# Performance work log

Measured on AMD Instinct MI355X. Metric: run time of the kernel, lower is better.

## Reference

```python
import jax, jax.numpy as jnp
import numpy as np

EMBED_DIM = 1024
NUM_HEADS = 16
HEAD_DIM = EMBED_DIM // NUM_HEADS


def setup_inputs() -> dict:
    key = jax.random.key(0)
    k_x, k_wqkv, k_bqkv, k_wout, k_bout = jax.random.split(key, 5)
    s = 1.0 / np.sqrt(EMBED_DIM)
    return {
        "x": jax.random.normal(k_x, (2, 2048, EMBED_DIM), dtype=jnp.float32),
        "w_qkv": jax.random.uniform(k_wqkv, (EMBED_DIM, 3 * EMBED_DIM), jnp.float32, -s, s),
        "b_qkv": jax.random.uniform(k_bqkv, (3 * EMBED_DIM,), jnp.float32, -s, s),
        "w_out": jax.random.uniform(k_wout, (EMBED_DIM, EMBED_DIM), jnp.float32, -s, s),
        "b_out": jax.random.uniform(k_bout, (EMBED_DIM,), jnp.float32, -s, s),
    }


def reference(x, w_qkv, b_qkv, w_out, b_out):
    B, S, D = x.shape
    H, Hd = NUM_HEADS, HEAD_DIM
    # qkv projection, then per-head chunk: layout matches torch view(B,S,H,3*Hd).chunk(3,-1)
    qkv = (x @ w_qkv + b_qkv).reshape(B, S, H, 3, Hd)  # [B,S,H,3,Hd]
    q = qkv[..., 0, :]  # [B,S,H,Hd]
    k = qkv[..., 1, :]
    v = qkv[..., 2, :]
    scale = 1.0 / np.sqrt(Hd).astype(np.float32)
    scores = jnp.einsum("bqhd,bkhd->bhqk", q, k) * scale  # [B,H,S,S]
    probs = jax.nn.softmax(scores, axis=-1)
    out = jnp.einsum("bhqk,bkhd->bqhd", probs, v).reshape(B, S, D)
    return out @ w_out + b_out
```

## Files before the change

### kernel.cpp

```cpp
#include <hip/hip_runtime.h>
#include <hip/hip_bf16.h>


typedef __bf16 bf16;
typedef __bf16 bf16x8 __attribute__((ext_vector_type(8)));
typedef float  f32x4  __attribute__((ext_vector_type(4)));
typedef float  f32x16 __attribute__((ext_vector_type(16)));
typedef unsigned int uint;
typedef unsigned int uint2v __attribute__((ext_vector_type(2)));

__device__ __forceinline__ void gload_lds16(const void* g, void* l) {
  __builtin_amdgcn_global_load_lds(
      (const __attribute__((address_space(1))) unsigned int*)g,
      (__attribute__((address_space(3))) unsigned int*)l, 16, 0, 0);
}

__device__ __forceinline__ uint pkbf16(float lo, float hi) {
  union { bf16 h[2]; uint u; } t;
  t.h[0] = (bf16)lo; t.h[1] = (bf16)hi;
  return t.u;
}

__device__ __forceinline__ void pl32swapu(uint& a, uint& b) {
  uint2v r = __builtin_amdgcn_permlane32_swap(a, b, false, false);
  a = r.x; b = r.y;
}
__device__ __forceinline__ void pl32swapf(float& a, float& b) {
  uint ua = __builtin_bit_cast(uint, a), ub = __builtin_bit_cast(uint, b);
  pl32swapu(ua, ub);
  a = __builtin_bit_cast(float, ua); b = __builtin_bit_cast(float, ub);
}

__global__ __launch_bounds__(256) void k_prep(const float* __restrict__ x,
                                              const float* __restrict__ w_qkv,
                                              const float* __restrict__ w_out,
                                              bf16* __restrict__ xb,
                                              bf16* __restrict__ wqT,
                                              bf16* __restrict__ woT) {
  __shared__ float tile[32][33];
  const int b = blockIdx.x;
  const int tid = threadIdx.x;
  if (b < 2048) {
    int i = (b * 256 + tid) * 8;
    float4 a = *(const float4*)(x + i);
    float4 c = *(const float4*)(x + i + 4);
    bf16x8 o;
    o[0] = (bf16)a.x; o[1] = (bf16)a.y; o[2] = (bf16)a.z; o[3] = (bf16)a.w;
    o[4] = (bf16)c.x; o[5] = (bf16)c.y; o[6] = (bf16)c.z; o[7] = (bf16)c.w;
    *(bf16x8*)(xb + i) = o;
    return;
  }
  const bool perm = (b < 5120);
  const float* in = perm ? w_qkv : w_out;
  bf16* out = perm ? wqT : woT;
  const int N = perm ? 3072 : 1024;
  int idx = perm ? (b - 2048) : (b - 5120);
  int gx = perm ? (idx % 96) : (idx % 32);
  int gy = perm ? (idx / 96) : (idx / 32);
  int n0 = gx * 32, k0 = gy * 32;
  int tx = tid & 31, ty = tid >> 5;
#pragma unroll
  for (int i = 0; i < 4; i++)
    tile[ty + i * 8][tx] = in[(size_t)(k0 + ty + i * 8) * N + n0 + tx];
  __syncthreads();
#pragma unroll
  for (int i = 0; i < 4; i++) {
    int n = n0 + ty + i * 8;
    int row = n;
    if (perm) {
      int rem = n % 192;
      row = (rem >> 6) * 1024 + (n / 192) * 64 + (rem & 63);
    }
    out[(size_t)row * 1024 + k0 + tx] = (bf16)tile[tx][ty + i * 8];
  }
}

template<int BM, int BN>
__device__ __forceinline__ void gemm_tile(const bf16* __restrict__ A, const bf16* __restrict__ B,
                                          int K, int m0, int n0,
                                          bf16* As, bf16* Bs, f32x4 acc[BM / 32][BN / 32]) {
  const int tid  = threadIdx.x;
  const int lane = tid & 63;
  const int wr   = (tid >> 7) & 1;
  const int wc   = (tid >> 6) & 1;
  constexpr int LA = BM / 64, LB = BN / 64;
  auto stage = [&](int k0v, int b) {
#pragma unroll
    for (int i = 0; i < LA; i++) {
      int row = i * 64 + (tid >> 2);
      int sw  = (tid & 3) ^ (row & 3);
      gload_lds16(A + (size_t)(m0 + row) * K + k0v + sw * 8, (char*)As + b * (BM * 64) + i * 4096 + tid * 16);
    }
#pragma unroll
    for (int i = 0; i < LB; i++) {
      int row = i * 64 + (tid >> 2);
      int sw  = (tid & 3) ^ (row & 3);
      gload_lds16(B + (size_t)(n0 + row) * K + k0v + sw * 8, (char*)Bs + b * (BN * 64) + i * 4096 + tid * 16);
    }
  };
  const int nk = K / 32;
  stage(0, 0); stage(32, 1); stage(64, 2);
  for (int t = 0; t < nk; t++) {
    if (t < nk - 2) {
      if constexpr (LA + LB == 4) asm volatile("s_waitcnt vmcnt(8)" ::: "memory");
      else                        asm volatile("s_waitcnt vmcnt(6)" ::: "memory");
    } else if (t < nk - 1) {
      if constexpr (LA + LB == 4) asm volatile("s_waitcnt vmcnt(4)" ::: "memory");
      else                        asm volatile("s_waitcnt vmcnt(3)" ::: "memory");
    } else {
      asm volatile("s_waitcnt vmcnt(0)" ::: "memory");
    }
    __builtin_amdgcn_s_barrier();
    asm volatile("" ::: "memory");
    if (t + 3 < nk) stage((t + 3) * 32, (t + 3) & 3);
    const int cur = t & 3;
    bf16x8 af[BM / 32], bfr[BN / 32];
#pragma unroll
    for (int r = 0; r < BM / 32; r++) {
      int ra = wr * (BM / 2) + r * 16 + (lane & 15);
      af[r]  = *(const bf16x8*)((const char*)As + cur * (BM * 64) + ra * 64 + ((((lane >> 4) << 4)) ^ ((ra & 3) << 4)));
    }
#pragma unroll
    for (int c = 0; c < BN / 32; c++) {
      int rb = wc * (BN / 2) + c * 16 + (lane & 15);
      bfr[c] = *(const bf16x8*)((const char*)Bs + cur * (BN * 64) + rb * 64 + ((((lane >> 4) << 4)) ^ ((rb & 3) << 4)));
    }
#pragma unroll
    for (int r = 0; r < BM / 32; r++)
#pragma unroll
      for (int c = 0; c < BN / 32; c++)
        acc[r][c] = __builtin_amdgcn_mfma_f32_16x16x32_bf16(af[r], bfr[c], acc[r][c], 0, 0, 0);
    asm volatile("" ::: "memory");
  }
}

__global__ __launch_bounds__(512, 2) void k_gemm_qkv(const bf16* __restrict__ A, const bf16* __restrict__ Bt,
                                                     const float* __restrict__ bias,
                                                     bf16* __restrict__ qb, bf16* __restrict__ kb,
                                                     bf16* __restrict__ vtb) {
  __shared__ char GS[131072];
  const int tid  = threadIdx.x;
  const int lane = tid & 63;
  const int wave = tid >> 6;
  const int wr   = wave >> 2;
  const int wc   = wave & 3;
  const int l = blockIdx.x;
  const int swz = (l & 7) * 24 + (l >> 3);
  const int m0 = (swz / 12) * 256, n0 = (swz % 12) * 256;
  const int K = 1024;

  f32x4 acc[8][4];
  f32x4 zero = {0.f, 0.f, 0.f, 0.f};
#pragma unroll
  for (int ms = 0; ms < 8; ms++)
#pragma unroll
    for (int ns = 0; ns < 4; ns++) acc[ms][ns] = zero;

  const int ccs = tid & 7;
  int rA[2], rB[2];
  {
    int lr0 = tid >> 3;
    rA[0] = lr0;
    rB[0] = (lr0 & 31) + ((lr0 >> 5) << 6);
    int lr1 = 64 + lr0;
    rA[1] = (lr1 & 63) + 128;
    rB[1] = (lr1 & 31) + ((lr1 >> 5) << 6);
  }
  const bf16* Agp[2]; const bf16* Bgp[2];
  int Alo[2], Blo[2];
#pragma unroll
  for (int j = 0; j < 2; j++) {
    Agp[j] = A  + (size_t)(m0 + rA[j]) * K + (ccs ^ (rA[j] & 7)) * 8;
    Alo[j] = rA[j] * 128 + ccs * 16;
    Bgp[j] = Bt + (size_t)(n0 + rB[j]) * K + (ccs ^ (rB[j] & 7)) * 8;
    Blo[j] = rB[j] * 128 + ccs * 16;
  }
  auto stA = [&](int t, int h) {
    int b = t & 1;
#pragma unroll
    for (int j = 0; j < 2; j++)
      gload_lds16(Agp[j] + (size_t)(h * 64) * K + t * 64, GS + b * 32768 + Alo[j] + h * 8192);
  };
  auto stB = [&](int t, int h) {
    int b = t & 1;
#pragma unroll
    for (int j = 0; j < 2; j++)
      gload_lds16(Bgp[j] + (size_t)(h * 32) * K + t * 64, GS + 65536 + b * 32768 + Blo[j] + h * 4096);
  };

  bf16x8 af[4][2], bf0[2][2], bf1[2][2];
  auto rdA = [&](const char* Ab, int mh) {
#pragma unroll
    for (int ms = 0; ms < 4; ms++)
#pragma unroll
      for (int ks = 0; ks < 2; ks++) {
        int row = wr * 128 + (mh * 4 + ms) * 16 + (lane & 15);
        int ch = (ks * 4 + (lane >> 4)) ^ (row & 7);
        af[ms][ks] = *(const bf16x8*)(Ab + row * 128 + ch * 16);
      }
  };
  auto rdB = [&](const char* Bb, int nh, bf16x8 (&bfx)[2][2]) {
#pragma unroll
    for (int ns = 0; ns < 2; ns++)
#pragma unroll
      for (int ks = 0; ks < 2; ks++) {
        int row = wc * 64 + (nh * 2 + ns) * 16 + (lane & 15);
        int ch = (ks * 4 + (lane >> 4)) ^ (row & 7);
        bfx[ns][ks] = *(const bf16x8*)(Bb + row * 128 + ch * 16);
      }
  };
  auto mm = [&](int mh, int nh, bf16x8 (&bfx)[2][2]) {
    __builtin_amdgcn_s_setprio(1);
#pragma unroll
    for (int ks = 0; ks < 2; ks++)
#pragma unroll
      for (int ms = 0; ms < 4; ms++)
#pragma unroll
        for (int ns = 0; ns < 2; ns++)
          acc[mh * 4 + ms][nh * 2 + ns] =
              __builtin_amdgcn_mfma_f32_16x16x32_bf16(af[ms][ks], bfx[ns][ks],
                                                      acc[mh * 4 + ms][nh * 2 + ns], 0, 0, 0);
    __builtin_amdgcn_s_setprio(0);
  };

#define BARRIER do { asm volatile("" ::: "memory"); __builtin_amdgcn_s_barrier(); \
                     asm volatile("" ::: "memory"); } while (0)

  stA(0, 0); stB(0, 0); stB(0, 1); stA(0, 1);
  stA(1, 0); stB(1, 0); stB(1, 1);
  asm volatile("s_waitcnt vmcnt(6)" ::: "memory");
  __builtin_amdgcn_s_barrier();
  asm volatile("" ::: "memory");

  for (int I = 0; I < 8; I++) {
    const int T = 2 * I;
    const char* Ab0 = GS;
    const char* Bb0 = GS + 65536;
    const char* Ab1 = GS + 32768;
    const char* Bb1 = GS + 65536 + 32768;
    const bool m2 = (T + 2 < 16), m3 = (T + 3 < 16);

    rdA(Ab0, 0); rdB(Bb0, 0, bf0);
    stA(T + 1, 1);
    BARRIER;
    mm(0, 0, bf0);

    rdB(Bb0, 1, bf1);
    if (m2) stA(T + 2, 0);
    BARRIER;
    mm(0, 1, bf1);

    rdA(Ab0, 1);
    if (m2) stB(T + 2, 0);
    BARRIER;
    mm(1, 0, bf0);

    if (m2) {
      stB(T + 2, 1);
      asm volatile("s_waitcnt vmcnt(6)" ::: "memory");
    } else {
      asm volatile("s_waitcnt vmcnt(0)" ::: "memory");
    }
    __builtin_amdgcn_s_barrier();
    asm volatile("" ::: "memory");
    mm(1, 1, bf1);

    rdA(Ab1, 0); rdB(Bb1, 0, bf0);
    if (m2) stA(T + 2, 1);
    BARRIER;
    mm(0, 0, bf0);

    rdB(Bb1, 1, bf1);
    if (m3) stA(T + 3, 0);
    BARRIER;
    mm(0, 1, bf1);

    rdA(Ab1, 1);
    if (m3) stB(T + 3, 0);
    BARRIER;
    mm(1, 0, bf0);

    if (m3) {
      stB(T + 3, 1);
      asm volatile("s_waitcnt vmcnt(6)" ::: "memory");
    } else {
      asm volatile("s_waitcnt vmcnt(0)" ::: "memory");
    }
    __builtin_amdgcn_s_barrier();
    asm volatile("" ::: "memory");
    mm(1, 1, bf1);
  }
#undef BARRIER

  const int group = n0 >> 10;
  const int hb = (n0 & 1023) >> 6;
  const int b_ = m0 >> 11;
  const float QSs = 0.125f * 1.4426950408889634f;
  char* TL = GS;

  if (group < 2) {
#pragma unroll
    for (int ms = 0; ms < 8; ms++) {
      int mloc = wr * 128 + ms * 16 + ((lane >> 4) << 2);
#pragma unroll
      for (int ns = 0; ns < 4; ns++) {
        int nloc = wc * 64 + ns * 16 + (lane & 15);
        int np = n0 + nloc;
        float bv = bias[((np & 1023) >> 6) * 192 + group * 64 + (np & 63)];
#pragma unroll
        for (int g = 0; g < 4; g++) {
          float v = acc[ms][ns][g] + bv;
          if (group == 0) v *= QSs;
          int m = mloc + g;
          int byte = m * 512 + ((((nloc >> 3) ^ (m & 7)) << 4) | ((nloc & 7) << 1));
          *(bf16*)(TL + byte) = (bf16)v;
        }
      }
    }
    __syncthreads();
    bf16* dst = (group == 0) ? qb : kb;
#pragma unroll
    for (int it = 0; it < 16; it++) {
      int cid = it * 512 + tid;
      int row = cid >> 5, cc = cid & 31;
      int hh = hb + (cc >> 3), ck = cc & 7;
      bf16x8 v8 = *(const bf16x8*)(TL + row * 512 + ((cc ^ (row & 7)) << 4));
      *(bf16x8*)(dst + ((size_t)(b_ * 16 + hh) * 2048 + (m0 & 2047) + row) * 64 + ck * 8) = v8;
    }
  } else {
#pragma unroll
    for (int ms = 0; ms < 8; ms++) {
      int mloc = wr * 128 + ms * 16 + ((lane >> 4) << 2);
#pragma unroll
      for (int ns = 0; ns < 4; ns++) {
        int nloc = wc * 64 + ns * 16 + (lane & 15);
        int np = n0 + nloc;
        float bv = bias[((np & 1023) >> 6) * 192 + 2 * 64 + (np & 63)];
#pragma unroll
        for (int g = 0; g < 4; g++) {
          float v = acc[ms][ns][g] + bv;
          int m = mloc + g;
          int byte = nloc * 512 + ((((m >> 3) ^ (nloc & 7)) << 4) | ((m & 7) << 1));
          *(bf16*)(TL + byte) = (bf16)v;
        }
      }
    }
    __syncthreads();
#pragma unroll
    for (int it = 0; it < 16; it++) {
      int cid = it * 512 + tid;
      int row = cid >> 5, mc = cid & 31;
      int hh = hb + (row >> 6), dd = row & 63;
      bf16x8 v8 = *(const bf16x8*)(TL + row * 512 + ((mc ^ (row & 7)) << 4));
      *(bf16x8*)(vtb + ((size_t)(b_ * 16 + hh) * 64 + dd) * 2048 + (m0 & 2047) + mc * 8) = v8;
    }
  }
}

__global__ __launch_bounds__(256) void k_gemm_out(const bf16* __restrict__ A, const bf16* __restrict__ Bt,
                                                  const float* __restrict__ bias,
                                                  float* __restrict__ out) {
  __shared__ bf16 As[4 * 64 * 32];
  __shared__ bf16 Bs[4 * 128 * 32];
  const int l = blockIdx.x;
  const int swz = (l & 7) * 64 + (l >> 3);
  int m0 = (swz >> 3) * 64, n0 = (swz & 7) * 128;
  f32x4 zero = {0.f, 0.f, 0.f, 0.f};
  f32x4 acc[2][4];
#pragma unroll
  for (int r = 0; r < 2; r++)
#pragma unroll
    for (int c = 0; c < 4; c++) acc[r][c] = zero;
  gemm_tile<64, 128>(A, Bt, 1024, m0, n0, As, Bs, acc);
  const int lane = threadIdx.x & 63;
  const int wr = (threadIdx.x >> 7) & 1, wc = (threadIdx.x >> 6) & 1;
#pragma unroll
  for (int r = 0; r < 2; r++) {
    int mbase = m0 + wr * 32 + r * 16 + ((lane >> 4) << 2);
#pragma unroll
    for (int c = 0; c < 4; c++) {
      int n = n0 + wc * 64 + c * 16 + (lane & 15);
      float bv = bias[n];
#pragma unroll
      for (int g = 0; g < 4; g++)
        out[(size_t)(mbase + g) * 1024 + n] = acc[r][c][g] + bv;
    }
  }
}

__global__ __launch_bounds__(512, 2) void k_attn(const bf16* __restrict__ qb, const bf16* __restrict__ kb,
                                                 const bf16* __restrict__ vtb, bf16* __restrict__ ob) {
  __shared__ char SMEM[147456];
  const int tid  = threadIdx.x;
  const int lane = tid & 63;
  const int wave = tid >> 6;
  const int qp   = wave & 3;
  const int half = wave >> 2;
  const int ln31 = lane & 31;
  const int g    = lane >> 5;

  int l = blockIdx.x;
  int x = l & 7, j = l >> 3;
  int qt = j & 7;
  int bh = x * 4 + (j >> 3);

  const int q0 = qt * 256 + qp * 64;

  bf16x8 qfa[4], qfb[4];
  {
    const bf16* qpa = qb + ((size_t)bh * 2048 + q0 + ln31) * 64 + g * 8;
    const bf16* qpb = qb + ((size_t)bh * 2048 + q0 + 32 + ln31) * 64 + g * 8;
#pragma unroll
    for (int dc = 0; dc < 4; dc++) {
      qfa[dc] = *(const bf16x8*)(qpa + dc * 16);
      qfb[dc] = *(const bf16x8*)(qpb + dc * 16);
    }
  }

  const f32x16 z16 = 0.f;
  f32x16 Oa0 = 0.f, Oa1 = 0.f, Ob0 = 0.f, Ob1 = 0.f;
  float lacc_a[4] = {0.f, 0.f, 0.f, 0.f};
  float lacc_b[4] = {0.f, 0.f, 0.f, 0.f};

  const int rbo = ln31 * 144 + (g << 4);
  const char* kbs = SMEM + half * 9216 + rbo;
  const char* vbs = SMEM + 18432 + half * 9216 + rbo;

  const int c1 = tid, r1 = c1 / 9, cc1 = c1 % 9;
  const int of1 = (cc1 == 8 ? 0 : cc1) * 8;
  const bf16* kg0a = kb  + ((size_t)bh * 2048 +        r1) * 64 + of1;
  const bf16* kg1a = kb  + ((size_t)bh * 2048 + 1024 + r1) * 64 + of1;
  const bf16* vg0a = vtb + ((size_t)bh * 64 + r1) * 2048 +        of1;
  const bf16* vg1a = vtb + ((size_t)bh * 64 + r1) * 2048 + 1024 + of1;
  const int se = tid >> 6;
  const int ce = 512 + (tid & 63), re = ce / 9, cce = ce % 9;
  const int ofe = (cce == 8 ? 0 : cce) * 8;
  const bf16* gext =
      (se == 0) ? kb  + ((size_t)bh * 2048 +        re) * 64 + ofe :
      (se == 1) ? kb  + ((size_t)bh * 2048 + 1024 + re) * 64 + ofe :
      (se == 2) ? vtb + ((size_t)bh * 64 + re) * 2048 +        ofe :
                  vtb + ((size_t)bh * 64 + re) * 2048 + 1024 + ofe;
  const size_t gadv = (se < 2) ? 4096 : 64;
  const int eoff = se * 9216 + ce * 16;

  auto stage = [&](int t, int s) {
    char* bs = SMEM + s * 36864;
    gload_lds16(kg0a + (size_t)t * 4096, bs +         c1 * 16);
    gload_lds16(kg1a + (size_t)t * 4096, bs + 9216  + c1 * 16);
    gload_lds16(vg0a + t * 64,           bs + 18432 + c1 * 16);
    gload_lds16(vg1a + t * 64,           bs + 27648 + c1 * 16);
    if (tid < 256) gload_lds16(gext + (size_t)t * gadv, bs + eoff);
  };

  auto smx = [&](f32x16& sv, bf16x8& f0, bf16x8& f1, float (&lc)[4]) {
#pragma unroll
    for (int r = 0; r < 16; r++) sv[r] = __builtin_amdgcn_exp2f(sv[r]);
#pragma unroll
    for (int r = 0; r < 4; r++)
      lc[r] += (sv[r] + sv[r + 4]) + (sv[r + 8] + sv[r + 12]);
    uint a0 = pkbf16(sv[0], sv[1]), a1 = pkbf16(sv[2], sv[3]);
    uint a2 = pkbf16(sv[4], sv[5]), a3 = pkbf16(sv[6], sv[7]);
    pl32swapu(a0, a2); pl32swapu(a1, a3);
    union { uint w[4]; bf16x8 v; } pa;
    pa.w[0] = a0; pa.w[1] = a1; pa.w[2] = a2; pa.w[3] = a3;
    f0 = pa.v;
    uint b0 = pkbf16(sv[8], sv[9]),  b1 = pkbf16(sv[10], sv[11]);
    uint b2 = pkbf16(sv[12], sv[13]), b3 = pkbf16(sv[14], sv[15]);
    pl32swapu(b0, b2); pl32swapu(b1, b3);
    union { uint w[4]; bf16x8 v; } pb;
    pb.w[0] = b0; pb.w[1] = b1; pb.w[2] = b2; pb.w[3] = b3;
    f1 = pb.v;
  };

  auto pv_chunk = [&](const char* Vb, int cb, bf16x8 f0a, bf16x8 f1a, bf16x8 f0b, bf16x8 f1b) {
    bf16x8 v0 = *(const bf16x8*)(Vb + cb);
    bf16x8 v1 = *(const bf16x8*)(Vb + 4608 + cb);
    Oa0 = __builtin_amdgcn_mfma_f32_32x32x16_bf16(v0, f0a, Oa0, 0, 0, 0);
    Ob0 = __builtin_amdgcn_mfma_f32_32x32x16_bf16(v0, f0b, Ob0, 0, 0, 0);
    Oa1 = __builtin_amdgcn_mfma_f32_32x32x16_bf16(v1, f0a, Oa1, 0, 0, 0);
    Ob1 = __builtin_amdgcn_mfma_f32_32x32x16_bf16(v1, f0b, Ob1, 0, 0, 0);
    v0 = *(const bf16x8*)(Vb + cb + 32);
    v1 = *(const bf16x8*)(Vb + 4608 + cb + 32);
    Oa0 = __builtin_amdgcn_mfma_f32_32x32x16_bf16(v0, f1a, Oa0, 0, 0, 0);
    Ob0 = __builtin_amdgcn_mfma_f32_32x32x16_bf16(v0, f1b, Ob0, 0, 0, 0);
    Oa1 = __builtin_amdgcn_mfma_f32_32x32x16_bf16(v1, f1a, Oa1, 0, 0, 0);
    Ob1 = __builtin_amdgcn_mfma_f32_32x32x16_bf16(v1, f1b, Ob1, 0, 0, 0);
  };

  bf16x8 hf0a, hf1a, hf0b, hf1b;

  stage(0, 0);
  stage(1, 1);
  for (int t = 0; t < 16; t++) {
    if (t + 1 < 16) {
      if (wave < 4) asm volatile("s_waitcnt vmcnt(5)" ::: "memory");
      else          asm volatile("s_waitcnt vmcnt(4)" ::: "memory");
    } else {
      asm volatile("s_waitcnt vmcnt(0)" ::: "memory");
    }
    __builtin_amdgcn_s_barrier();
    asm volatile("" ::: "memory");
    if (t + 2 < 16) stage(t + 2, (t + 2) & 3);

    const char* Kb = kbs + (t & 3) * 36864;
    const char* Vb = vbs + (t & 3) * 36864;

    if (half && t) {
      const char* Vp = vbs + ((t + 3) & 3) * 36864;
      __builtin_amdgcn_s_setprio(1);
      pv_chunk(Vp, 64, hf0a, hf1a, hf0b, hf1b);
      __builtin_amdgcn_s_setprio(0);
    }

    f32x16 sAa, sAb, sBa, sBb;
    __builtin_amdgcn_s_setprio(1);
    {
      bf16x8 kA = *(const bf16x8*)(Kb + 0);
      bf16x8 kB = *(const bf16x8*)(Kb + 4608);
      sAa = __builtin_amdgcn_mfma_f32_32x32x16_bf16(kA, qfa[0], z16, 0, 0, 0);
      sAb = __builtin_amdgcn_mfma_f32_32x32x16_bf16(kA, qfb[0], z16, 0, 0, 0);
      sBa = __builtin_amdgcn_mfma_f32_32x32x16_bf16(kB, qfa[0], z16, 0, 0, 0);
      sBb = __builtin_amdgcn_mfma_f32_32x32x16_bf16(kB, qfb[0], z16, 0, 0, 0);
    }
#pragma unroll
    for (int dc = 1; dc < 4; dc++) {
      bf16x8 kA = *(const bf16x8*)(Kb + dc * 32);
      bf16x8 kB = *(const bf16x8*)(Kb + 4608 + dc * 32);
      sAa = __builtin_amdgcn_mfma_f32_32x32x16_bf16(kA, qfa[dc], sAa, 0, 0, 0);
      sAb = __builtin_amdgcn_mfma_f32_32x32x16_bf16(kA, qfb[dc], sAb, 0, 0, 0);
      sBa = __builtin_amdgcn_mfma_f32_32x32x16_bf16(kB, qfa[dc], sBa, 0, 0, 0);
      sBb = __builtin_amdgcn_mfma_f32_32x32x16_bf16(kB, qfb[dc], sBb, 0, 0, 0);
    }
    __builtin_amdgcn_s_setprio(0);

    bf16x8 fa0, fa1, fb0, fb1;
    smx(sAa, fa0, fa1, lacc_a);
    smx(sAb, fb0, fb1, lacc_b);
    __builtin_amdgcn_s_setprio(1);
    pv_chunk(Vb, 0, fa0, fa1, fb0, fb1);
    __builtin_amdgcn_s_setprio(0);
    if (half) {
      smx(sBa, hf0a, hf1a, lacc_a);
      smx(sBb, hf0b, hf1b, lacc_b);
    } else {
      smx(sBa, fa0, fa1, lacc_a);
      smx(sBb, fb0, fb1, lacc_b);
      __builtin_amdgcn_s_setprio(1);
      pv_chunk(Vb, 64, fa0, fa1, fb0, fb1);
      __builtin_amdgcn_s_setprio(0);
    }
    asm volatile("" ::: "memory");
  }
  if (half) {
    pv_chunk(vbs + 3 * 36864, 64, hf0a, hf1a, hf0b, hf1b);
  }

  float l_ra = (lacc_a[0] + lacc_a[1]) + (lacc_a[2] + lacc_a[3]);
  { float o = l_ra; pl32swapf(l_ra, o); l_ra += o; }
  float l_rb = (lacc_b[0] + lacc_b[1]) + (lacc_b[2] + lacc_b[3]);
  { float o = l_rb; pl32swapf(l_rb, o); l_rb += o; }

  float* Opart = (float*)SMEM;
  float* LsA   = (float*)(SMEM + 69632);
  float* LsB   = (float*)(SMEM + 70144);
  __syncthreads();
  if (half == 1) {
    float* my = Opart + (qp * 64 + lane) * 68;
#pragma unroll
    for (int c = 0; c < 4; c++) {
      *(f32x4*)(my +      c * 4) = f32x4{Oa0[c*4], Oa0[c*4+1], Oa0[c*4+2], Oa0[c*4+3]};
      *(f32x4*)(my + 16 + c * 4) = f32x4{Oa1[c*4], Oa1[c*4+1], Oa1[c*4+2], Oa1[c*4+3]};
      *(f32x4*)(my + 32 + c * 4) = f32x4{Ob0[c*4], Ob0[c*4+1], Ob0[c*4+2], Ob0[c*4+3]};
      *(f32x4*)(my + 48 + c * 4) = f32x4{Ob1[c*4], Ob1[c*4+1], Ob1[c*4+2], Ob1[c*4+3]};
    }
    if (lane < 32) { LsA[qp * 32 + ln31] = l_ra; LsB[qp * 32 + ln31] = l_rb; }
  }
  __syncthreads();
  float inva = 0.f, invb = 0.f;
  if (half == 0) {
    const float* pr = Opart + (qp * 64 + lane) * 68;
#pragma unroll
    for (int c = 0; c < 4; c++) {
      f32x4 a0 = *(const f32x4*)(pr +      c * 4);
      f32x4 a1 = *(const f32x4*)(pr + 16 + c * 4);
      f32x4 b0 = *(const f32x4*)(pr + 32 + c * 4);
      f32x4 b1 = *(const f32x4*)(pr + 48 + c * 4);
#pragma unroll
      for (int k = 0; k < 4; k++) {
        Oa0[c*4+k] += a0[k]; Oa1[c*4+k] += a1[k];
        Ob0[c*4+k] += b0[k]; Ob1[c*4+k] += b1[k];
      }
    }
    inva = 1.0f / (l_ra + LsA[qp * 32 + ln31]);
    invb = 1.0f / (l_rb + LsB[qp * 32 + ln31]);
  }
  __syncthreads();
  bf16 (*Os)[64][72] = reinterpret_cast<bf16 (*)[64][72]>(SMEM);
  if (half == 0) {
#pragma unroll
    for (int r = 0; r < 16; r++) {
      int d0 = (r & 3) + 8 * (r >> 2) + 4 * g;
      Os[qp][ln31][d0]           = (bf16)(Oa0[r] * inva);
      Os[qp][ln31][d0 + 32]      = (bf16)(Oa1[r] * inva);
      Os[qp][32 + ln31][d0]      = (bf16)(Ob0[r] * invb);
      Os[qp][32 + ln31][d0 + 32] = (bf16)(Ob1[r] * invb);
    }
  }
  __syncthreads();
  {
    int b_ = bh >> 4, h = bh & 15;
#pragma unroll
    for (int it = 0; it < 4; it++) {
      int cid = it * 512 + tid;
      int row256 = cid >> 3, c = cid & 7;
      int qpp = row256 >> 6, row = row256 & 63;
      bf16x8 v8o = *(const bf16x8*)&Os[qpp][row][c * 8];
      *(bf16x8*)(ob + ((size_t)(b_ * 2048 + qt * 256 + qpp * 64 + row)) * 1024 + h * 64 + c * 8) = v8o;
    }
  }
}

extern "C" void kernel_launch(void* const* d_in, const int* in_sizes, int n_in,
                              void* d_out, int out_size, void* d_ws, size_t ws_size,
                              hipStream_t stream) {
  const float* x     = (const float*)d_in[0];
  const float* w_qkv = (const float*)d_in[1];
  const float* b_qkv = (const float*)d_in[2];
  const float* w_out = (const float*)d_in[3];
  const float* b_out = (const float*)d_in[4];
  float* out = (float*)d_out;

  char* ws = (char*)d_ws;
  bf16* xb  = (bf16*)ws;
  bf16* wqT = (bf16*)(ws + (8ull  << 20));
  bf16* woT = (bf16*)(ws + (14ull << 20));
  bf16* qb  = (bf16*)(ws + (16ull << 20));
  bf16* kb  = (bf16*)(ws + (24ull << 20));
  bf16* vtb = (bf16*)(ws + (32ull << 20));

  k_prep<<<6144, 256, 0, stream>>>(x, w_qkv, w_out, xb, wqT, woT);
  k_gemm_qkv<<<192, 512, 0, stream>>>(xb, wqT, b_qkv, qb, kb, vtb);
  k_attn<<<256, 512, 0, stream>>>(qb, kb, vtb, xb);
  k_gemm_out<<<512, 256, 0, stream>>>(xb, woT, b_out, out);
}
```

Before: 104.7 us.

## Store K/V in MFMA fragment order and load directly from global in attention

```diff
diff --git a/kernel.cpp b/kernel.cpp
--- a/kernel.cpp
+++ b/kernel.cpp
@@ -136,8 +136,8 @@
 
 __global__ __launch_bounds__(512, 2) void k_gemm_qkv(const bf16* __restrict__ A, const bf16* __restrict__ Bt,
                                                      const float* __restrict__ bias,
-                                                     bf16* __restrict__ qb, bf16* __restrict__ kb,
-                                                     bf16* __restrict__ vtb) {
+                                                     bf16* __restrict__ qb, char* __restrict__ kf,
+                                                     char* __restrict__ vf) {
   __shared__ char GS[131072];
   const int tid  = threadIdx.x;
   const int lane = tid & 63;
@@ -295,6 +295,7 @@
   const int group = n0 >> 10;
   const int hb = (n0 & 1023) >> 6;
   const int b_ = m0 >> 11;
+  const int kt0 = (m0 & 2047) >> 5;
   const float QSs = 0.125f * 1.4426950408889634f;
   char* TL = GS;
 
@@ -318,14 +319,30 @@
       }
     }
     __syncthreads();
-    bf16* dst = (group == 0) ? qb : kb;
-#pragma unroll
-    for (int it = 0; it < 16; it++) {
-      int cid = it * 512 + tid;
-      int row = cid >> 5, cc = cid & 31;
-      int hh = hb + (cc >> 3), ck = cc & 7;
-      bf16x8 v8 = *(const bf16x8*)(TL + row * 512 + ((cc ^ (row & 7)) << 4));
-      *(bf16x8*)(dst + ((size_t)(b_ * 16 + hh) * 2048 + (m0 & 2047) + row) * 64 + ck * 8) = v8;
+    if (group == 0) {
+#pragma unroll
+      for (int it = 0; it < 16; it++) {
+        int cid = it * 512 + tid;
+        int row = cid >> 5, cc = cid & 31;
+        int hh = hb + (cc >> 3), ck = cc & 7;
+        bf16x8 v8 = *(const bf16x8*)(TL + row * 512 + ((cc ^ (row & 7)) << 4));
+        *(bf16x8*)(qb + ((size_t)(b_ * 16 + hh) * 2048 + (m0 & 2047) + row) * 64 + ck * 8) = v8;
+      }
+    } else {
+#pragma unroll
+      for (int it = 0; it < 16; it++) {
+        int cid = it * 512 + tid;
+        int hh = cid >> 11;
+        int ktl = (cid >> 8) & 7;
+        int dc = (cid >> 6) & 3;
+        int gg = (cid >> 5) & 1;
+        int ln = cid & 31;
+        int row = ktl * 32 + ln;
+        int cc = hh * 8 + dc * 2 + gg;
+        bf16x8 v8 = *(const bf16x8*)(TL + row * 512 + ((cc ^ (row & 7)) << 4));
+        *(bf16x8*)(kf + ((size_t)(b_ * 16 + hb + hh) * 64 + kt0 + ktl) * 4096
+                      + (dc * 2 + gg) * 512 + ln * 16) = v8;
+      }
     }
   } else {
 #pragma unroll
@@ -349,10 +366,17 @@
 #pragma unroll
     for (int it = 0; it < 16; it++) {
       int cid = it * 512 + tid;
-      int row = cid >> 5, mc = cid & 31;
-      int hh = hb + (row >> 6), dd = row & 63;
+      int hh = cid >> 11;
+      int ktl = (cid >> 8) & 7;
+      int kc = (cid >> 7) & 1;
+      int dt = (cid >> 6) & 1;
+      int gg = (cid >> 5) & 1;
+      int ln = cid & 31;
+      int row = hh * 64 + dt * 32 + ln;
+      int mc = ktl * 4 + kc * 2 + gg;
       bf16x8 v8 = *(const bf16x8*)(TL + row * 512 + ((mc ^ (row & 7)) << 4));
-      *(bf16x8*)(vtb + ((size_t)(b_ * 16 + hh) * 64 + dd) * 2048 + (m0 & 2047) + mc * 8) = v8;
+      *(bf16x8*)(vf + ((size_t)(b_ * 16 + hb + hh) * 64 + kt0 + ktl) * 4096
+                    + ((kc * 2 + dt) * 2 + gg) * 512 + ln * 16) = v8;
     }
   }
 }
@@ -388,9 +412,9 @@
   }
 }
 
-__global__ __launch_bounds__(512, 2) void k_attn(const bf16* __restrict__ qb, const bf16* __restrict__ kb,
-                                                 const bf16* __restrict__ vtb, bf16* __restrict__ ob) {
-  __shared__ char SMEM[147456];
+__global__ __launch_bounds__(512, 2) void k_attn(const bf16* __restrict__ qb, const char* __restrict__ kf,
+                                                 const char* __restrict__ vf, bf16* __restrict__ ob) {
+  __shared__ char SMEM[73728];
   const int tid  = threadIdx.x;
   const int lane = tid & 63;
   const int wave = tid >> 6;
@@ -422,35 +446,9 @@
   float lacc_a[4] = {0.f, 0.f, 0.f, 0.f};
   float lacc_b[4] = {0.f, 0.f, 0.f, 0.f};
 
-  const int rbo = ln31 * 144 + (g << 4);
-  const char* kbs = SMEM + half * 9216 + rbo;
-  const char* vbs = SMEM + 18432 + half * 9216 + rbo;
-
-  const int c1 = tid, r1 = c1 / 9, cc1 = c1 % 9;
-  const int of1 = (cc1 == 8 ? 0 : cc1) * 8;
-  const bf16* kg0a = kb  + ((size_t)bh * 2048 +        r1) * 64 + of1;
-  const bf16* kg1a = kb  + ((size_t)bh * 2048 + 1024 + r1) * 64 + of1;
-  const bf16* vg0a = vtb + ((size_t)bh * 64 + r1) * 2048 +        of1;
-  const bf16* vg1a = vtb + ((size_t)bh * 64 + r1) * 2048 + 1024 + of1;
-  const int se = tid >> 6;
-  const int ce = 512 + (tid & 63), re = ce / 9, cce = ce % 9;
-  const int ofe = (cce == 8 ? 0 : cce) * 8;
-  const bf16* gext =
-      (se == 0) ? kb  + ((size_t)bh * 2048 +        re) * 64 + ofe :
-      (se == 1) ? kb  + ((size_t)bh * 2048 + 1024 + re) * 64 + ofe :
-      (se == 2) ? vtb + ((size_t)bh * 64 + re) * 2048 +        ofe :
-                  vtb + ((size_t)bh * 64 + re) * 2048 + 1024 + ofe;
-  const size_t gadv = (se < 2) ? 4096 : 64;
-  const int eoff = se * 9216 + ce * 16;
-
-  auto stage = [&](int t, int s) {
-    char* bs = SMEM + s * 36864;
-    gload_lds16(kg0a + (size_t)t * 4096, bs +         c1 * 16);
-    gload_lds16(kg1a + (size_t)t * 4096, bs + 9216  + c1 * 16);
-    gload_lds16(vg0a + t * 64,           bs + 18432 + c1 * 16);
-    gload_lds16(vg1a + t * 64,           bs + 27648 + c1 * 16);
-    if (tid < 256) gload_lds16(gext + (size_t)t * gadv, bs + eoff);
-  };
+  const int lb = (g * 32 + ln31) * 16;
+  const char* Kp = kf + (size_t)bh * 262144 + (half * 32) * 4096 + lb;
+  const char* Vp = vf + (size_t)bh * 262144 + (half * 32) * 4096 + lb;
 
   auto smx = [&](f32x16& sv, bf16x8& f0, bf16x8& f1, float (&lc)[4]) {
 #pragma unroll
@@ -472,87 +470,49 @@
     f1 = pb.v;
   };
 
-  auto pv_chunk = [&](const char* Vb, int cb, bf16x8 f0a, bf16x8 f1a, bf16x8 f0b, bf16x8 f1b) {
-    bf16x8 v0 = *(const bf16x8*)(Vb + cb);
-    bf16x8 v1 = *(const bf16x8*)(Vb + 4608 + cb);
-    Oa0 = __builtin_amdgcn_mfma_f32_32x32x16_bf16(v0, f0a, Oa0, 0, 0, 0);
-    Ob0 = __builtin_amdgcn_mfma_f32_32x32x16_bf16(v0, f0b, Ob0, 0, 0, 0);
-    Oa1 = __builtin_amdgcn_mfma_f32_32x32x16_bf16(v1, f0a, Oa1, 0, 0, 0);
-    Ob1 = __builtin_amdgcn_mfma_f32_32x32x16_bf16(v1, f0b, Ob1, 0, 0, 0);
-    v0 = *(const bf16x8*)(Vb + cb + 32);
-    v1 = *(const bf16x8*)(Vb + 4608 + cb + 32);
-    Oa0 = __builtin_amdgcn_mfma_f32_32x32x16_bf16(v0, f1a, Oa0, 0, 0, 0);
-    Ob0 = __builtin_amdgcn_mfma_f32_32x32x16_bf16(v0, f1b, Ob0, 0, 0, 0);
-    Oa1 = __builtin_amdgcn_mfma_f32_32x32x16_bf16(v1, f1a, Oa1, 0, 0, 0);
-    Ob1 = __builtin_amdgcn_mfma_f32_32x32x16_bf16(v1, f1b, Ob1, 0, 0, 0);
-  };
-
-  bf16x8 hf0a, hf1a, hf0b, hf1b;
-
-  stage(0, 0);
-  stage(1, 1);
-  for (int t = 0; t < 16; t++) {
-    if (t + 1 < 16) {
-      if (wave < 4) asm volatile("s_waitcnt vmcnt(5)" ::: "memory");
-      else          asm volatile("s_waitcnt vmcnt(4)" ::: "memory");
-    } else {
-      asm volatile("s_waitcnt vmcnt(0)" ::: "memory");
-    }
-    __builtin_amdgcn_s_barrier();
-    asm volatile("" ::: "memory");
-    if (t + 2 < 16) stage(t + 2, (t + 2) & 3);
-
-    const char* Kb = kbs + (t & 3) * 36864;
-    const char* Vb = vbs + (t & 3) * 36864;
-
-    if (half && t) {
-      const char* Vp = vbs + ((t + 3) & 3) * 36864;
-      __builtin_amdgcn_s_setprio(1);
-      pv_chunk(Vp, 64, hf0a, hf1a, hf0b, hf1b);
-      __builtin_amdgcn_s_setprio(0);
-    }
-
-    f32x16 sAa, sAb, sBa, sBb;
+  bf16x8 k0 = *(const bf16x8*)(Kp +    0);
+  bf16x8 k1 = *(const bf16x8*)(Kp + 1024);
+  bf16x8 k2 = *(const bf16x8*)(Kp + 2048);
+  bf16x8 k3 = *(const bf16x8*)(Kp + 3072);
+
+  for (int ss = 0; ss < 32; ss++, Kp += 4096, Vp += 4096) {
+    bf16x8 v00 = *(const bf16x8*)(Vp +    0);
+    bf16x8 v01 = *(const bf16x8*)(Vp + 1024);
+    bf16x8 v10 = *(const bf16x8*)(Vp + 2048);
+    bf16x8 v11 = *(const bf16x8*)(Vp + 3072);
+    bf16x8 n0 = *(const bf16x8*)(Kp + 4096);
+    bf16x8 n1 = *(const bf16x8*)(Kp + 5120);
+    bf16x8 n2 = *(const bf16x8*)(Kp + 6144);
+    bf16x8 n3 = *(const bf16x8*)(Kp + 7168);
+
+    f32x16 sa, sb;
     __builtin_amdgcn_s_setprio(1);
-    {
-      bf16x8 kA = *(const bf16x8*)(Kb + 0);
-      bf16x8 kB = *(const bf16x8*)(Kb + 4608);
-      sAa = __builtin_amdgcn_mfma_f32_32x32x16_bf16(kA, qfa[0], z16, 0, 0, 0);
-      sAb = __builtin_amdgcn_mfma_f32_32x32x16_bf16(kA, qfb[0], z16, 0, 0, 0);
-      sBa = __builtin_amdgcn_mfma_f32_32x32x16_bf16(kB, qfa[0], z16, 0, 0, 0);
-      sBb = __builtin_amdgcn_mfma_f32_32x32x16_bf16(kB, qfb[0], z16, 0, 0, 0);
-    }
-#pragma unroll
-    for (int dc = 1; dc < 4; dc++) {
-      bf16x8 kA = *(const bf16x8*)(Kb + dc * 32);
-      bf16x8 kB = *(const bf16x8*)(Kb + 4608 + dc * 32);
-      sAa = __builtin_amdgcn_mfma_f32_32x32x16_bf16(kA, qfa[dc], sAa, 0, 0, 0);
-      sAb = __builtin_amdgcn_mfma_f32_32x32x16_bf16(kA, qfb[dc], sAb, 0, 0, 0);
-      sBa = __builtin_amdgcn_mfma_f32_32x32x16_bf16(kB, qfa[dc], sBa, 0, 0, 0);
-      sBb = __builtin_amdgcn_mfma_f32_32x32x16_bf16(kB, qfb[dc], sBb, 0, 0, 0);
-    }
+    sa = __builtin_amdgcn_mfma_f32_32x32x16_bf16(k0, qfa[0], z16, 0, 0, 0);
+    sb = __builtin_amdgcn_mfma_f32_32x32x16_bf16(k0, qfb[0], z16, 0, 0, 0);
+    sa = __builtin_amdgcn_mfma_f32_32x32x16_bf16(k1, qfa[1], sa, 0, 0, 0);
+    sb = __builtin_amdgcn_mfma_f32_32x32x16_bf16(k1, qfb[1], sb, 0, 0, 0);
+    sa = __builtin_amdgcn_mfma_f32_32x32x16_bf16(k2, qfa[2], sa, 0, 0, 0);
+    sb = __builtin_amdgcn_mfma_f32_32x32x16_bf16(k2, qfb[2], sb, 0, 0, 0);
+    sa = __builtin_amdgcn_mfma_f32_32x32x16_bf16(k3, qfa[3], sa, 0, 0, 0);
+    sb = __builtin_amdgcn_mfma_f32_32x32x16_bf16(k3, qfb[3], sb, 0, 0, 0);
     __builtin_amdgcn_s_setprio(0);
 
     bf16x8 fa0, fa1, fb0, fb1;
-    smx(sAa, fa0, fa1, lacc_a);
-    smx(sAb, fb0, fb1, lacc_b);
+    smx(sa, fa0, fa1, lacc_a);
+    smx(sb, fb0, fb1, lacc_b);
+
     __builtin_amdgcn_s_setprio(1);
-    pv_chunk(Vb, 0, fa0, fa1, fb0, fb1);
+    Oa0 = __builtin_amdgcn_mfma_f32_32x32x16_bf16(v00, fa0, Oa0, 0, 0, 0);
+    Ob0 = __builtin_amdgcn_mfma_f32_32x32x16_bf16(v00, fb0, Ob0, 0, 0, 0);
+    Oa1 = __builtin_amdgcn_mfma_f32_32x32x16_bf16(v01, fa0, Oa1, 0, 0, 0);
+    Ob1 = __builtin_amdgcn_mfma_f32_32x32x16_bf16(v01, fb0, Ob1, 0, 0, 0);
+    Oa0 = __builtin_amdgcn_mfma_f32_32x32x16_bf16(v10, fa1, Oa0, 0, 0, 0);
+    Ob0 = __builtin_amdgcn_mfma_f32_32x32x16_bf16(v10, fb1, Ob0, 0, 0, 0);
+    Oa1 = __builtin_amdgcn_mfma_f32_32x32x16_bf16(v11, fa1, Oa1, 0, 0, 0);
+    Ob1 = __builtin_amdgcn_mfma_f32_32x32x16_bf16(v11, fb1, Ob1, 0, 0, 0);
     __builtin_amdgcn_s_setprio(0);
-    if (half) {
-      smx(sBa, hf0a, hf1a, lacc_a);
-      smx(sBb, hf0b, hf1b, lacc_b);
-    } else {
-      smx(sBa, fa0, fa1, lacc_a);
-      smx(sBb, fb0, fb1, lacc_b);
-      __builtin_amdgcn_s_setprio(1);
-      pv_chunk(Vb, 64, fa0, fa1, fb0, fb1);
-      __builtin_amdgcn_s_setprio(0);
-    }
-    asm volatile("" ::: "memory");
-  }
-  if (half) {
-    pv_chunk(vbs + 3 * 36864, 64, hf0a, hf1a, hf0b, hf1b);
+
+    k0 = n0; k1 = n1; k2 = n2; k3 = n3;
   }
 
   float l_ra = (lacc_a[0] + lacc_a[1]) + (lacc_a[2] + lacc_a[3]);
@@ -635,11 +595,11 @@
   bf16* wqT = (bf16*)(ws + (8ull  << 20));
   bf16* woT = (bf16*)(ws + (14ull << 20));
   bf16* qb  = (bf16*)(ws + (16ull << 20));
-  bf16* kb  = (bf16*)(ws + (24ull << 20));
-  bf16* vtb = (bf16*)(ws + (32ull << 20));
+  char* kf  = ws + (24ull << 20);
+  char* vf  = ws + (32ull << 20);
 
   k_prep<<<6144, 256, 0, stream>>>(x, w_qkv, w_out, xb, wqT, woT);
-  k_gemm_qkv<<<192, 512, 0, stream>>>(xb, wqT, b_qkv, qb, kb, vtb);
-  k_attn<<<256, 512, 0, stream>>>(qb, kb, vtb, xb);
+  k_gemm_qkv<<<192, 512, 0, stream>>>(xb, wqT, b_qkv, qb, kf, vf);
+  k_attn<<<256, 512, 0, stream>>>(qb, kf, vf, xb);
   k_gemm_out<<<512, 256, 0, stream>>>(xb, woT, b_out, out);
 }
```

Result: no change. 103.6 us, median of 2 (-1.0%).
